# Optimization experiments

Hardware: AMD Instinct MI355X
Metric: run time of the kernel (lower is better)

## Reference

```python
import jax, jax.numpy as jnp
import numpy as np

N = 50000        # nodes
E = 600000       # edges (avg degree 12)
NODE, EDGE, GDIM = 15, 10, 8
HID, L, H = 128, 3, 4
D = HID // H     # per-head dim = 32


def setup_inputs() -> dict:
    key = jax.random.key(0)
    ks = jax.random.split(key, 32)
    f = lambda i, shape, s=0.05: jax.random.normal(ks[i], shape, dtype=jnp.float32) * s
    return {
        "x": f(0, (N, NODE), 1.0),
        "edge_index": jax.random.randint(ks[1], (2, E), 0, N, dtype=jnp.int32),
        "edge_attr": f(2, (E, EDGE), 1.0),
        "u": f(3, (GDIM,), 1.0),
        "enc_w": f(4, (NODE, HID)), "enc_b": f(5, (HID,)),
        "gat_lin_w": f(6, (L, HID, HID)),
        "gat_att_src": f(7, (L, H, D)), "gat_att_dst": f(8, (L, H, D)),
        "gat_lin_edge": f(9, (L, EDGE, HID)), "gat_att_edge": f(10, (L, H, D)),
        "gat_bias": f(11, (L, HID)),
        "ln_g": jnp.ones((L, HID), jnp.float32), "ln_b": jnp.zeros((L, HID), jnp.float32),
        "pool_w": f(12, (3 * HID + GDIM, GDIM)), "pool_b": f(13, (GDIM,)),
        "pool_ln_g": jnp.ones((GDIM,), jnp.float32), "pool_ln_b": jnp.zeros((GDIM,), jnp.float32),
        "head_w1": f(14, (4, HID, 32)), "head_b1": f(15, (4, 32)),
        "head_w2": f(16, (4, 32, 1)), "head_b2": f(17, (4, 1)),
        "strat_w1": f(18, (HID, 32)), "strat_b1": f(19, (32,)),
        "strat_w2": f(20, (32, 5)), "strat_b2": f(21, (5,)),
        "glob_w1": f(22, (GDIM, 32)), "glob_b1": f(23, (32,)),
        "glob_w2": f(24, (32, 4)), "glob_b2": f(25, (4,)),
    }


def _layer_norm(x, g, b, eps=1e-5):
    mu = jnp.mean(x, axis=-1, keepdims=True)
    var = jnp.mean(jnp.square(x - mu), axis=-1, keepdims=True)
    return (x - mu) * jax.lax.rsqrt(var + eps) * g + b


def _forward(edge_index, x, edge_attr, u, enc_w, enc_b, gat_lin_w, gat_att_src,
             gat_att_dst, gat_lin_edge, gat_att_edge, gat_bias, ln_g, ln_b,
             pool_w, pool_b, pool_ln_g, pool_ln_b, head_w1, head_b1, head_w2,
             head_b2, strat_w1, strat_b1, strat_w2, strat_b2, glob_w1, glob_b1,
             glob_w2, glob_b2):
    src0, dst0 = edge_index[0], edge_index[1]
    # PyG GATConv add_self_loops=True with fill_value='mean': self-loop edge
    # attr for node i = mean of edge_attr over edges whose dst is i.
    cnt = jax.ops.segment_sum(jnp.ones((E,), jnp.float32), dst0, num_segments=N)
    ea_self = jax.ops.segment_sum(edge_attr, dst0, num_segments=N) / jnp.maximum(cnt, 1.0)[:, None]
    loop = jnp.arange(N, dtype=src0.dtype)
    src = jnp.concatenate([src0, loop])
    dst = jnp.concatenate([dst0, loop])
    ea = jnp.concatenate([edge_attr, ea_self], axis=0)   # [E+N, EDGE]

    h = jax.nn.relu(x @ enc_w + enc_b)                   # node encoder [N, HID]
    for l in range(L):
        hp = (h @ gat_lin_w[l]).reshape(N, H, D)         # projected nodes
        a_s = jnp.sum(hp * gat_att_src[l], axis=-1)      # [N, H]
        a_d = jnp.sum(hp * gat_att_dst[l], axis=-1)
        ep = (ea @ gat_lin_edge[l]).reshape(-1, H, D)    # [E+N, H, D]
        a_e = jnp.sum(ep * gat_att_edge[l], axis=-1)     # [E+N, H]
        alpha = jax.nn.leaky_relu(a_s[src] + a_d[dst] + a_e, negative_slope=0.2)
        # numerically-stable softmax over incoming edges per dst node
        m = jax.ops.segment_max(alpha, dst, num_segments=N)
        w = jnp.exp(alpha - m[dst])
        denom = jax.ops.segment_sum(w, dst, num_segments=N)
        attn = w / denom[dst]                            # every node has a self-loop
        out = jax.ops.segment_sum(hp[src] * attn[..., None], dst, num_segments=N)
        out = out.reshape(N, HID) + gat_bias[l]
        # residual (shapes match) + dropout(eval=id) + layer norm
        h = _layer_norm(h + out, ln_g[l], ln_b[l])

    pooled = jnp.concatenate([h.mean(0), h.max(0), h.sum(0), u])[None]  # [1, 3*HID+GDIM]
    g = _layer_norm(jax.nn.relu(pooled @ pool_w + pool_b), pool_ln_g, pool_ln_b)

    # four stacked 128->32->1 heads (priority:tanh, coop/urgency/safety:sigmoid)
    z = jax.nn.relu(jnp.einsum('nf,kfh->knh', h, head_w1) + head_b1[:, None, :])
    y = jnp.einsum('knh,kho->kno', z, head_w2) + head_b2[:, None, :]   # [4, N, 1]
    priority = jnp.tanh(y[0])
    cooperation = jax.nn.sigmoid(y[1])
    urgency = jax.nn.sigmoid(y[2])
    safety = jax.nn.sigmoid(y[3])
    strategies = jax.nn.softmax(jax.nn.relu(h @ strat_w1 + strat_b1) @ strat_w2 + strat_b2, axis=-1)
    global_signal = jnp.tanh(jax.nn.relu(g @ glob_w1 + glob_b1) @ glob_w2 + glob_b2)[0]  # [4]
    return (priority, cooperation, urgency, safety, strategies, global_signal)


def reference(x, edge_index, edge_attr, u, enc_w, enc_b, gat_lin_w, gat_att_src,
              gat_att_dst, gat_lin_edge, gat_att_edge, gat_bias, ln_g, ln_b,
              pool_w, pool_b, pool_ln_g, pool_ln_b, head_w1, head_b1, head_w2,
              head_b2, strat_w1, strat_b1, strat_w2, strat_b2, glob_w1, glob_b1,
              glob_w2, glob_b2):
    return _forward(edge_index, x, edge_attr, u, enc_w, enc_b, gat_lin_w,
                    gat_att_src, gat_att_dst, gat_lin_edge, gat_att_edge,
                    gat_bias, ln_g, ln_b, pool_w, pool_b, pool_ln_g, pool_ln_b,
                    head_w1, head_b1, head_w2, head_b2, strat_w1, strat_b1,
                    strat_w2, strat_b2, glob_w1, glob_b1, glob_w2, glob_b2)
```

## Files before the change

kernel.cpp:

```cpp
#include <hip/hip_runtime.h>
#include <hip/hip_bf16.h>
#include <hip/hip_fp16.h>

#define N_NODES 50000
#define N_EDGES 600000
#define TOT_E   (N_EDGES + N_NODES)
#define NLAYER  3
#define PB      200
#define SCB     512
#define NSB     ((N_NODES + SCB - 1)/SCB)
#define CAP     96

typedef __hip_bfloat16 bf16;
typedef __attribute__((ext_vector_type(8))) short short8;
typedef __attribute__((ext_vector_type(4))) float floatx4;

__device__ __forceinline__ float b2f(bf16 v){ return __bfloat162float(v); }

__device__ __forceinline__ float ldm(const void* p, long i, int m){
  return m ? ((const float*)p)[i] : b2f(((const bf16*)p)[i]);
}

__device__ __forceinline__ unsigned bfr(float f){
  unsigned u = __float_as_uint(f);
  return (u + 0x7fffu + ((u>>16)&1u)) >> 16;
}
__device__ __forceinline__ void splitbf(float f, ushort& hi, ushort& lo){
  unsigned hb = bfr(f);
  float fh = __uint_as_float(hb<<16);
  hi = (ushort)hb;
  lo = (ushort)bfr(f - fh);
}
__device__ __forceinline__ float unpk(ushort hi, ushort lo){
  return __uint_as_float((unsigned)hi<<16) + __uint_as_float((unsigned)lo<<16);
}

__global__ void detect_kernel(const void* probe, int* mode){
  __shared__ float red[256];
  int t = threadIdx.x;
  const bf16* p = (const bf16*)probe;
  float mx = 0.f;
  for (int i = t; i < 1920; i += 256){
    float v = fabsf(b2f(p[i]));
    if (!isfinite(v)) v = 1e30f;
    mx = fmaxf(mx, v);
  }
  red[t] = mx; __syncthreads();
  if (t == 0){
    float m = 0.f;
    for (int i = 0; i < 256; i++) m = fmaxf(m, red[i]);
    mode[0] = (m > 1000.0f) ? 1 : 0;
  }
}

__global__ void sentinel_kernel(int host_code, float* out){
  if (threadIdx.x == 0 && blockIdx.x == 0) out[0] = (float)host_code;
}

struct CvtTab { const void* s[27]; float* d[27]; int n[27]; };
__global__ void cvt_small_kernel(CvtTab tab, const int* mode){
  int b = blockIdx.x;
  int i = blockIdx.y*256 + threadIdx.x;
  if (i < tab.n[b]) tab.d[b][i] = ldm(tab.s[b], i, mode[0]);
}

__global__ void prep_kernel(const float* __restrict__ Wl, const float* __restrict__ att_src,
                            const float* __restrict__ att_dst, const float* __restrict__ head_w1,
                            const float* __restrict__ strat_w1, const float* __restrict__ head_b1,
                            const float* __restrict__ strat_b1, const float* __restrict__ lin_e,
                            const float* __restrict__ att_edge,
                            ushort* __restrict__ Bsw0, ushort* __restrict__ Bsw1,
                            float* __restrict__ b1cat, float* __restrict__ Mmat){
  int tid = blockIdx.x*256 + threadIdx.x;
  if (tid < 3*4*144*32){
    int l = tid / 18432, rr = tid % 18432;
    int kt = rr / 4608, r2 = rr % 4608;
    int n = r2 / 32, kk = r2 & 31;
    int k = kt*32 + kk;
    float f;
    if (n < 128)      f = Wl[l*16384 + k*128 + n];
    else if (n < 136){
      int c = n - 128, sd = c >> 2, hh = c & 3;
      const float* w = Wl + l*16384 + k*128 + hh*32;
      const float* a = (sd ? att_dst : att_src) + l*128 + hh*32;
      float s = 0;
      #pragma unroll
      for (int d = 0; d < 32; d++) s += w[d]*a[d];
      f = s;
    } else f = 0.f;
    ushort hb, lb; splitbf(f, hb, lb);
    Bsw0[(size_t)(l*2+0)*18432 + kt*4608 + n*32 + kk] = hb;
    Bsw0[(size_t)(l*2+1)*18432 + kt*4608 + n*32 + kk] = lb;
  } else if (tid < 3*4*144*32 + 4*160*32){
    int t2 = tid - 3*4*144*32;
    int kt = t2 / 5120, r2 = t2 % 5120;
    int n = r2 / 32, kk = r2 & 31;
    int k = kt*32 + kk;
    float f = (n < 128) ? head_w1[(n>>5)*4096 + k*32 + (n&31)]
                        : strat_w1[k*32 + (n-128)];
    ushort hb, lb; splitbf(f, hb, lb);
    Bsw1[kt*5120 + n*32 + kk]          = hb;
    Bsw1[4*5120 + kt*5120 + n*32 + kk] = lb;
  } else if (tid < 75936){
    int c = tid - 75776;
    b1cat[c] = (c < 128) ? head_b1[c] : strat_b1[c-128];
  } else if (tid < 76056){
    int t = tid - 75936;
    int l = t / 40, r = t % 40, k = r / 4, hh = r % 4;
    float s = 0;
    #pragma unroll
    for (int d = 0; d < 32; d++)
      s += lin_e[l*1280 + k*128 + hh*32 + d] * att_edge[l*128 + hh*32 + d];
    Mmat[t] = s;
  }
}

__global__ void count_kernel(const int* __restrict__ ei, int* __restrict__ cnt, int* devflags){
  int e = blockIdx.x*256 + threadIdx.x;
  if (e >= N_EDGES) return;
  int s = ei[e], d = ei[N_EDGES + e];
  if (((unsigned)s >= N_NODES) || ((unsigned)d >= N_NODES)) atomicOr(&devflags[0], 1);
  else atomicAdd(&cnt[d], 1);
  if (e < 1024 && ei[2*e + 1] == 0) atomicAdd(&devflags[1], 1);
}

__global__ __launch_bounds__(SCB) void scan1_kernel(const int* __restrict__ cnt, int* __restrict__ bsum){
  __shared__ int ws[SCB/64];
  int i = blockIdx.x*SCB + threadIdx.x;
  int v = (i < N_NODES) ? cnt[i] + 1 : 0;
  int lane = threadIdx.x & 63, w = threadIdx.x >> 6;
  #pragma unroll
  for (int off = 1; off < 64; off <<= 1) v += __shfl_xor(v, off);
  if (lane == 0) ws[w] = v;
  __syncthreads();
  if (threadIdx.x == 0){
    int s = 0;
    #pragma unroll
    for (int k = 0; k < SCB/64; k++) s += ws[k];
    bsum[blockIdx.x] = s;
  }
}

__global__ __launch_bounds__(SCB) void scan3_kernel(const int* __restrict__ cnt, const int* __restrict__ bsum,
                                                    int* __restrict__ rowptr){
  __shared__ int sm[SCB];
  __shared__ int boff;
  int t = threadIdx.x;
  if (t < 64){
    int s = 0;
    for (int i = t; i < blockIdx.x; i += 64) s += bsum[i];
    #pragma unroll
    for (int off = 1; off < 64; off <<= 1) s += __shfl_xor(s, off);
    if (t == 0) boff = s;
  }
  int i = blockIdx.x*SCB + t;
  int v = (i < N_NODES) ? cnt[i] + 1 : 0;
  sm[t] = v; __syncthreads();
  for (int off = 1; off < SCB; off <<= 1){
    int add = (t >= off) ? sm[t-off] : 0;
    __syncthreads();
    sm[t] += add;
    __syncthreads();
  }
  if (i < N_NODES) rowptr[i] = boff + sm[t] - v;
  if (blockIdx.x == NSB-1 && t == SCB-1) rowptr[N_NODES] = boff + sm[SCB-1];
}

__global__ void scatter_ae_kernel(const int* __restrict__ ei, const void* __restrict__ ea_raw,
                                  const int* __restrict__ mode, const float* __restrict__ Mmat,
                                  const int* __restrict__ rowptr, int* __restrict__ fill,
                                  int* __restrict__ srcs, float4* __restrict__ aec){
  int e = blockIdx.x*256 + threadIdx.x;
  if (e >= TOT_E) return;
  if (e < N_EDGES){
    int s = ei[e], d = ei[N_EDGES + e];
    int pos = rowptr[d] + atomicAdd(&fill[d], 1);
    srcs[pos] = s;
    int m = mode[0];
    float v[10];
    #pragma unroll
    for (int k = 0; k < 10; k++) v[k] = ldm(ea_raw, (long)e*10 + k, m);
    #pragma unroll
    for (int l = 0; l < 3; l++){
      float r[4];
      #pragma unroll
      for (int hh = 0; hh < 4; hh++){
        float s2 = 0;
        #pragma unroll
        for (int k = 0; k < 10; k++) s2 += v[k]*Mmat[l*40 + k*4 + hh];
        r[hh] = s2;
      }
      aec[(size_t)l*TOT_E + pos] = make_float4(r[0], r[1], r[2], r[3]);
    }
  } else {
    int i = e - N_EDGES;
    srcs[rowptr[i+1] - 1] = i;
  }
}

__global__ __launch_bounds__(128) void encoder_kernel(const void* __restrict__ x_raw, const int* __restrict__ mode,
                                                      const float* __restrict__ enc_w, const float* __restrict__ enc_b,
                                                      ushort* __restrict__ h_hi, ushort* __restrict__ h_lo){
  __shared__ float xs[16];
  int n = blockIdx.x, j = threadIdx.x;
  if (j < 15) xs[j] = ldm(x_raw, (long)n*15 + j, mode[0]);
  __syncthreads();
  float acc = enc_b[j];
  #pragma unroll
  for (int k = 0; k < 15; k++) acc += xs[k] * enc_w[k*128 + j];
  acc = fmaxf(acc, 0.0f);
  ushort hi, lo; splitbf(acc, hi, lo);
  h_hi[(size_t)n*128 + j] = hi;
  h_lo[(size_t)n*128 + j] = lo;
}

template<int NT, int MODE>
__global__ __launch_bounds__(256) void gemm_mfma(
    const ushort* __restrict__ Ahi, const ushort* __restrict__ Alo,
    const ushort* __restrict__ Bhi, const ushort* __restrict__ Blo,
    int M, const float* __restrict__ bias, __half* __restrict__ Ch,
    float* __restrict__ a_s, float* __restrict__ a_d,
    const float* __restrict__ hw2, const float* __restrict__ hb2,
    const float* __restrict__ sw2, const float* __restrict__ sb2, float* __restrict__ out,
    const int* __restrict__ devflags, const int* __restrict__ mode){
  int wv = threadIdx.x >> 6, lane = threadIdx.x & 63;
  int nl = lane & 15, q = lane >> 4;
  int row0 = blockIdx.x*64 + wv*16;
  if (row0 >= M) return;
  floatx4 acc[NT];
  #pragma unroll
  for (int t = 0; t < NT; t++) acc[t] = (floatx4){0.f, 0.f, 0.f, 0.f};
  int ra = row0 + nl; if (ra > M-1) ra = M-1;
  const ushort* ah = Ahi + (size_t)ra*128 + q*8;
  const ushort* al = Alo + (size_t)ra*128 + q*8;
  #pragma unroll
  for (int kt = 0; kt < 4; kt++){
    short8 ahi = *(const short8*)(ah + kt*32);
    short8 alo = *(const short8*)(al + kt*32);
    const ushort* bh = Bhi + kt*(NT*16*32) + nl*32 + q*8;
    const ushort* bl = Blo + kt*(NT*16*32) + nl*32 + q*8;
    #pragma unroll
    for (int t = 0; t < NT; t++){
      short8 b0 = *(const short8*)(bh + t*512);
      short8 b1 = *(const short8*)(bl + t*512);
      acc[t] = __builtin_amdgcn_mfma_f32_16x16x32_bf16(ahi, b0, acc[t], 0, 0, 0);
      acc[t] = __builtin_amdgcn_mfma_f32_16x16x32_bf16(alo, b0, acc[t], 0, 0, 0);
      acc[t] = __builtin_amdgcn_mfma_f32_16x16x32_bf16(ahi, b1, acc[t], 0, 0, 0);
    }
  }
  if (MODE == 0){
    #pragma unroll
    for (int r = 0; r < 4; r++){
      int row = row0 + q*4 + r;
      if (row >= M) continue;
      #pragma unroll
      for (int t = 0; t < 8; t++)
        Ch[(size_t)row*128 + t*16 + nl] = __float2half(acc[t][r]);
      if (nl < 4)      a_s[row*4 + nl]       = acc[8][r];
      else if (nl < 8) a_d[row*4 + (nl - 4)] = acc[8][r];
    }
  } else {
    float b1v[NT], hw2v[8], sw2v[10];
    #pragma unroll
    for (int t = 0; t < NT; t++) b1v[t] = bias[t*16 + nl];
    #pragma unroll
    for (int t = 0; t < 8; t++) hw2v[t] = hw2[t*16 + nl];
    #pragma unroll
    for (int t = 0; t < 2; t++)
      #pragma unroll
      for (int j = 0; j < 5; j++) sw2v[t*5 + j] = sw2[(t*16 + nl)*5 + j];
    #pragma unroll
    for (int r = 0; r < 4; r++){
      int row = row0 + q*4 + r;
      float pk[4] = {0,0,0,0};
      float sv[5] = {0,0,0,0,0};
      #pragma unroll
      for (int t = 0; t < 8; t++){
        float z = fmaxf(acc[t][r] + b1v[t], 0.f);
        pk[t>>1] += z*hw2v[t];
      }
      #pragma unroll
      for (int t = 0; t < 2; t++){
        float z = fmaxf(acc[8+t][r] + b1v[8+t], 0.f);
        #pragma unroll
        for (int j = 0; j < 5; j++) sv[j] += z*sw2v[t*5 + j];
      }
      #pragma unroll
      for (int off = 1; off <= 8; off <<= 1){
        #pragma unroll
        for (int k = 0; k < 4; k++) pk[k] += __shfl_xor(pk[k], off);
        #pragma unroll
        for (int j = 0; j < 5; j++) sv[j] += __shfl_xor(sv[j], off);
      }
      if (nl == 0 && row < M){
        float y0 = pk[0] + hb2[0];
        float y1 = pk[1] + hb2[1];
        float y2 = pk[2] + hb2[2];
        float y3 = pk[3] + hb2[3];
        float p0 = tanhf(y0);
        if (row == 0){
          int code = 0;
          if (devflags[1] > 900)      code = 16384;
          else if (devflags[0])       code = 20480;
          if (code) p0 = (float)(code + 512*mode[0]);
        }
        out[row]             = p0;
        out[N_NODES + row]   = 1.f/(1.f + __expf(-y1));
        out[2*N_NODES + row] = 1.f/(1.f + __expf(-y2));
        out[3*N_NODES + row] = 1.f/(1.f + __expf(-y3));
        float s5[5], mxs = -3.4e38f;
        #pragma unroll
        for (int j = 0; j < 5; j++){ s5[j] = sv[j] + sb2[j]; mxs = fmaxf(mxs, s5[j]); }
        float se = 0;
        #pragma unroll
        for (int j = 0; j < 5; j++){ s5[j] = __expf(s5[j] - mxs); se += s5[j]; }
        float inv = 1.f/se;
        #pragma unroll
        for (int j = 0; j < 5; j++) out[4*N_NODES + (size_t)row*5 + j] = s5[j]*inv;
      }
    }
  }
}

__global__ __launch_bounds__(256) void fused_agg_kernel(
    const __half* __restrict__ hp, const float* __restrict__ a_s, const float* __restrict__ a_d,
    const float* __restrict__ aecl, const int* __restrict__ srcs, const int* __restrict__ rowptr,
    const float* __restrict__ bias_l, const float* __restrict__ ln_g_l,
    const float* __restrict__ ln_b_l, ushort* __restrict__ h_hi, ushort* __restrict__ h_lo){
  __shared__ float wsm[4][CAP*4];
  __shared__ int   ssm[4][CAP];
  int wv = threadIdx.x >> 6;
  int n = blockIdx.x*4 + wv;
  int lane = threadIdx.x & 63;
  int p0 = rowptr[n], p1 = rowptr[n+1];
  int deg = p1 - p0 - 1;
  int hh = lane & 3;
  int esl = lane >> 2;
  float adv = a_d[n*4 + hh];
  float asn = a_s[n*4 + hh];
  bool fits = (deg <= CAP);

  float ls = 0.f, ssum = 0.f;
  for (int base = 0; base < deg; base += 16){
    int idx = base + esl;
    if (idx < deg){
      int p = p0 + idx;
      float aev = aecl[(size_t)p*4 + hh];
      int sv = srcs[p];
      float al = a_s[sv*4 + hh] + adv + aev;
      al = (al > 0.f) ? al : 0.2f*al;
      float e = __expf(al);
      ssum += aev; ls += e;
      if (fits){
        wsm[wv][idx*4 + hh] = e;
        if (hh == 0) ssm[wv][idx] = sv;
      }
    }
  }
  #pragma unroll
  for (int off = 4; off <= 32; off <<= 1){
    ls   += __shfl_xor(ls, off);
    ssum += __shfl_xor(ssum, off);
  }
  float aself = ssum / (float)(deg > 0 ? deg : 1);
  float als = asn + adv + aself;
  als = (als > 0.f) ? als : 0.2f*als;
  float es = __expf(als);
  float invd = 1.f/(ls + es);

  int hsel = lane >> 4;
  float invdh = __shfl(invd, hsel);
  float esh   = __shfl(es, hsel);

  float acc0 = 0.f, acc1 = 0.f;
  if (fits){
    for (int j = 0; j < deg; j++){
      float w = wsm[wv][j*4 + hsel]*invdh;
      int  sj = ssm[wv][j];
      __half2 hv = *((const __half2*)(hp + (size_t)sj*128) + lane);
      acc0 += w*__half2float(hv.x);
      acc1 += w*__half2float(hv.y);
    }
  } else {
    for (int base = 0; base < deg; base += 16){
      int idx = base + esl;
      float wgt = 0.f; int sv = 0;
      if (idx < deg){
        int p = p0 + idx;
        float aev = aecl[(size_t)p*4 + hh];
        sv = srcs[p];
        float al = a_s[sv*4 + hh] + adv + aev;
        al = (al > 0.f) ? al : 0.2f*al;
        wgt = __expf(al)*invd;
      }
      int cnt_e = min(16, deg - base);
      for (int j = 0; j < cnt_e; j++){
        float w = __shfl(wgt, j*4 + hsel);
        int  sj = __shfl(sv,  j*4);
        __half2 hv = *((const __half2*)(hp + (size_t)sj*128) + lane);
        acc0 += w*__half2float(hv.x);
        acc1 += w*__half2float(hv.y);
      }
    }
  }
  {
    float w = esh*invdh;
    __half2 hv = *((const __half2*)(hp + (size_t)n*128) + lane);
    acc0 += w*__half2float(hv.x);
    acc1 += w*__half2float(hv.y);
  }
  ushort2 rh = *(const ushort2*)(h_hi + (size_t)n*128 + lane*2);
  ushort2 rl = *(const ushort2*)(h_lo + (size_t)n*128 + lane*2);
  float2 bi  = *(const float2*)(bias_l + lane*2);
  float v0 = acc0 + bi.x + unpk(rh.x, rl.x);
  float v1 = acc1 + bi.y + unpk(rh.y, rl.y);
  float s = v0 + v1, sq = v0*v0 + v1*v1;
  #pragma unroll
  for (int off = 32; off >= 1; off >>= 1){ s += __shfl_xor(s, off); sq += __shfl_xor(sq, off); }
  float mu  = s * (1.0f/128.0f);
  float var = sq * (1.0f/128.0f) - mu*mu;
  float rs  = rsqrtf(fmaxf(var, 0.0f) + 1e-5f);
  float2 g  = *(const float2*)(ln_g_l + lane*2);
  float2 bb = *(const float2*)(ln_b_l + lane*2);
  float o0 = (v0 - mu)*rs*g.x + bb.x;
  float o1 = (v1 - mu)*rs*g.y + bb.y;
  ushort2 oh, ol;
  splitbf(o0, oh.x, ol.x);
  splitbf(o1, oh.y, ol.y);
  *(ushort2*)(h_hi + (size_t)n*128 + lane*2) = oh;
  *(ushort2*)(h_lo + (size_t)n*128 + lane*2) = ol;
}

__global__ __launch_bounds__(128) void pool_part_kernel(const ushort* __restrict__ h_hi,
                                                        const ushort* __restrict__ h_lo,
                                                        float* __restrict__ psum, float* __restrict__ pmax){
  int b = blockIdx.x, j = threadIdx.x;
  int nb = b*(N_NODES/PB), ne = nb + (N_NODES/PB);
  float s = 0, m = -3.4e38f;
  for (int n = nb; n < ne; n++){
    float v = unpk(h_hi[(size_t)n*128 + j], h_lo[(size_t)n*128 + j]);
    s += v; m = fmaxf(m, v);
  }
  psum[b*128 + j] = s; pmax[b*128 + j] = m;
}

__global__ __launch_bounds__(128) void global_kernel(
    const float* __restrict__ psum, const float* __restrict__ pmax,
    const float* __restrict__ u, const float* __restrict__ pool_w, const float* __restrict__ pool_b,
    const float* __restrict__ pool_ln_g, const float* __restrict__ pool_ln_b,
    const float* __restrict__ glob_w1, const float* __restrict__ glob_b1,
    const float* __restrict__ glob_w2, const float* __restrict__ glob_b2, float* __restrict__ out_glob){
  __shared__ float pooled[392];
  __shared__ float gv[8];
  __shared__ float t1[32];
  __shared__ float mv[2];
  int t = threadIdx.x;
  float s = 0, m = -3.4e38f;
  for (int b = 0; b < PB; b++){ s += psum[b*128 + t]; m = fmaxf(m, pmax[b*128 + t]); }
  pooled[t]       = s * (1.0f/(float)N_NODES);
  pooled[128 + t] = m;
  pooled[256 + t] = s;
  if (t < 8) pooled[384 + t] = u[t];
  __syncthreads();
  if (t < 8){
    float acc = pool_b[t];
    for (int f = 0; f < 392; f++) acc += pooled[f]*pool_w[f*8 + t];
    gv[t] = fmaxf(acc, 0.0f);
  }
  __syncthreads();
  if (t == 0){
    float mu = 0; for (int i = 0; i < 8; i++) mu += gv[i];
    mu *= 0.125f;
    float var = 0; for (int i = 0; i < 8; i++){ float d = gv[i]-mu; var += d*d; }
    var *= 0.125f;
    mv[0] = mu; mv[1] = rsqrtf(var + 1e-5f);
  }
  __syncthreads();
  float gnorm = (t < 8) ? (gv[t]-mv[0])*mv[1]*pool_ln_g[t] + pool_ln_b[t] : 0.0f;
  __syncthreads();
  if (t < 8) gv[t] = gnorm;
  __syncthreads();
  if (t < 32){
    float acc = glob_b1[t];
    for (int q = 0; q < 8; q++) acc += gv[q]*glob_w1[q*32 + t];
    t1[t] = fmaxf(acc, 0.0f);
  }
  __syncthreads();
  if (t < 4){
    float acc = glob_b2[t];
    for (int mm = 0; mm < 32; mm++) acc += t1[mm]*glob_w2[mm*4 + t];
    out_glob[t] = tanhf(acc);
  }
}

extern "C" void kernel_launch(void* const* d_in, const int* in_sizes, int n_in,
                              void* d_out, int out_size, void* d_ws, size_t ws_size,
                              hipStream_t stream){
  float* out = (float*)d_out;

  static const int exp_sizes[30] = {
    750000, 1200000, 6000000, 8, 1920, 128, 49152, 384, 384, 3840, 384,
    384, 384, 384, 3136, 8, 8, 8, 16384, 128, 128, 4, 4096, 32, 160, 5,
    256, 32, 128, 4 };
  int host_code = 0;
  if (n_in != 30){
    int nn = n_in < 0 ? 0 : (n_in > 63 ? 63 : n_in);
    host_code = 4096 + 32*nn;
  } else {
    for (int i = 0; i < 30; i++)
      if (in_sizes[i] != exp_sizes[i]){ host_code = 1024 + 8*i; break; }
  }
  if (!host_code && out_size != 9*N_NODES + 4) host_code = 12288;
  if (host_code){
    sentinel_kernel<<<1, 64, 0, stream>>>(host_code, out);
    return;
  }

  const int* ei = (const int*)d_in[1];

  char* wsp = (char*)d_ws;
  size_t off = 0;
  auto alloc = [&](size_t bytes)->char*{ char* p = wsp + off; off += (bytes + 255) & ~(size_t)255; return p; };

  ushort* h_hi = (ushort*)alloc((size_t)N_NODES*128*2);
  ushort* h_lo = (ushort*)alloc((size_t)N_NODES*128*2);
  __half* hp   = (__half*)alloc((size_t)N_NODES*128*2);
  float*  a_s  = (float*)alloc((size_t)N_NODES*4*4);
  float*  a_d  = (float*)alloc((size_t)N_NODES*4*4);
  float*  aec  = (float*)alloc((size_t)3*TOT_E*16);
  int*   srcs   = (int*)alloc((size_t)TOT_E*4);
  int*   rowptr = (int*)alloc((size_t)(N_NODES+1)*4);
  int*   bsum   = (int*)alloc((size_t)NSB*4);

  const int SN = 27;
  static const int sn_sizes[SN] = {
    8, 1920, 128, 49152, 384, 384, 3840, 384, 384, 384, 384,
    3136, 8, 8, 8, 16384, 128, 128, 4, 4096, 32, 160, 5, 256, 32, 128, 4 };
  static const int sn_input[SN] = {
    3, 4, 5, 6, 7, 8, 9, 10, 11, 12, 13, 14, 15, 16, 17,
    18, 19, 20, 21, 22, 23, 24, 25, 26, 27, 28, 29 };
  float* sarr[SN];
  for (int i = 0; i < SN; i++) sarr[i] = (float*)alloc((size_t)sn_sizes[i]*4);
  float* u_c       = sarr[0];
  float* enc_w_c   = sarr[1];
  float* enc_b_c   = sarr[2];
  float* Wl        = sarr[3];
  float* att_src_c = sarr[4];
  float* att_dst_c = sarr[5];
  float* lin_e_c   = sarr[6];
  float* att_e_c   = sarr[7];
  float* bias_c    = sarr[8];
  float* ln_g_c    = sarr[9];
  float* ln_b_c    = sarr[10];
  float* pool_w_c  = sarr[11];
  float* pool_b_c  = sarr[12];
  float* pln_g_c   = sarr[13];
  float* pln_b_c   = sarr[14];
  float* head_w1_c = sarr[15];
  float* head_b1_c = sarr[16];
  float* head_w2_c = sarr[17];
  float* head_b2_c = sarr[18];
  float* strat_w1_c= sarr[19];
  float* strat_b1_c= sarr[20];
  float* strat_w2_c= sarr[21];
  float* strat_b2_c= sarr[22];
  float* glob_w1_c = sarr[23];
  float* glob_b1_c = sarr[24];
  float* glob_w2_c = sarr[25];
  float* glob_b2_c = sarr[26];

  float*  b1cat = (float*)alloc(160*4);
  float*  Mmat  = (float*)alloc(3*40*4);
  ushort* Bsw0  = (ushort*)alloc((size_t)3*2*4*144*32*2);
  ushort* Bsw1  = (ushort*)alloc((size_t)2*4*160*32*2);
  int*    mode  = (int*)alloc(256);
  float*  psum  = (float*)alloc((size_t)PB*128*4);
  float*  pmax  = (float*)alloc((size_t)PB*128*4);
  size_t zero_begin = off;
  int*   devflags = (int*)alloc(256);
  int*   cnt      = (int*)alloc((size_t)N_NODES*4);
  int*   fill     = (int*)alloc((size_t)N_NODES*4);
  size_t zero_bytes = off - zero_begin;

  if (ws_size < off){
    sentinel_kernel<<<1, 64, 0, stream>>>(8192, out);
    return;
  }

  hipMemsetAsync(wsp + zero_begin, 0, zero_bytes, stream);

  detect_kernel<<<1, 256, 0, stream>>>(d_in[4], mode);

  CvtTab tab;
  for (int i = 0; i < SN; i++){ tab.s[i] = d_in[sn_input[i]]; tab.d[i] = sarr[i]; tab.n[i] = sn_sizes[i]; }
  cvt_small_kernel<<<dim3(SN, 192), 256, 0, stream>>>(tab, mode);

  prep_kernel<<<(76056 + 255)/256, 256, 0, stream>>>(Wl, att_src_c, att_dst_c, head_w1_c, strat_w1_c,
                                                     head_b1_c, strat_b1_c, lin_e_c, att_e_c,
                                                     Bsw0, Bsw1, b1cat, Mmat);
  count_kernel<<<(N_EDGES + 255)/256, 256, 0, stream>>>(ei, cnt, devflags);
  scan1_kernel<<<NSB, SCB, 0, stream>>>(cnt, bsum);
  scan3_kernel<<<NSB, SCB, 0, stream>>>(cnt, bsum, rowptr);
  scatter_ae_kernel<<<(TOT_E + 255)/256, 256, 0, stream>>>(ei, d_in[2], mode, Mmat, rowptr, fill,
                                                           srcs, (float4*)aec);
  encoder_kernel<<<N_NODES, 128, 0, stream>>>(d_in[0], mode, enc_w_c, enc_b_c, h_hi, h_lo);

  const int gb = (N_NODES + 63)/64;
  for (int l = 0; l < NLAYER; l++){
    const ushort* Bhi = Bsw0 + (size_t)l*2*18432;
    const ushort* Blo = Bhi + 18432;
    gemm_mfma<9,0><<<gb, 256, 0, stream>>>(h_hi, h_lo, Bhi, Blo, N_NODES, nullptr, hp, a_s, a_d,
                                           nullptr, nullptr, nullptr, nullptr, nullptr, nullptr, nullptr);
    fused_agg_kernel<<<N_NODES/4, 256, 0, stream>>>(hp, a_s, a_d, aec + (size_t)l*TOT_E*4, srcs, rowptr,
                                                    bias_c + l*128, ln_g_c + l*128, ln_b_c + l*128, h_hi, h_lo);
  }

  pool_part_kernel<<<PB, 128, 0, stream>>>(h_hi, h_lo, psum, pmax);
  global_kernel<<<1, 128, 0, stream>>>(psum, pmax, u_c, pool_w_c, pool_b_c, pln_g_c, pln_b_c,
                                       glob_w1_c, glob_b1_c, glob_w2_c, glob_b2_c, out + 9*N_NODES);
  gemm_mfma<10,1><<<gb, 256, 0, stream>>>(h_hi, h_lo, Bsw1, Bsw1 + 4*5120, N_NODES, b1cat, nullptr,
                                          nullptr, nullptr, head_w2_c, head_b2_c, strat_w2_c, strat_b2_c,
                                          out, devflags, mode);
}
```

Baseline: 498.1 us.

## Pack edge records with fp16 attrs and compute edge attention on the fly

```diff
diff --git a/kernel.cpp b/kernel.cpp
--- a/kernel.cpp
+++ b/kernel.cpp
@@ -33,6 +33,16 @@
 }
 __device__ __forceinline__ float unpk(ushort hi, ushort lo){
   return __uint_as_float((unsigned)hi<<16) + __uint_as_float((unsigned)lo<<16);
+}
+
+__device__ __forceinline__ float dot10(int4 r0, int4 r1, const float* Mv){
+  __half2 h; float2 f; float s = 0.f;
+  h = *(__half2*)&r0.y; f = __half22float2(h); s += f.x*Mv[0] + f.y*Mv[1];
+  h = *(__half2*)&r0.z; f = __half22float2(h); s += f.x*Mv[2] + f.y*Mv[3];
+  h = *(__half2*)&r0.w; f = __half22float2(h); s += f.x*Mv[4] + f.y*Mv[5];
+  h = *(__half2*)&r1.x; f = __half22float2(h); s += f.x*Mv[6] + f.y*Mv[7];
+  h = *(__half2*)&r1.y; f = __half22float2(h); s += f.x*Mv[8] + f.y*Mv[9];
+  return s;
 }
 
 __global__ void detect_kernel(const void* probe, int* mode){
@@ -166,36 +176,25 @@
   if (blockIdx.x == NSB-1 && t == SCB-1) rowptr[N_NODES] = boff + sm[SCB-1];
 }
 
-__global__ void scatter_ae_kernel(const int* __restrict__ ei, const void* __restrict__ ea_raw,
-                                  const int* __restrict__ mode, const float* __restrict__ Mmat,
-                                  const int* __restrict__ rowptr, int* __restrict__ fill,
-                                  int* __restrict__ srcs, float4* __restrict__ aec){
+__global__ void scatter_rec_kernel(const int* __restrict__ ei, const void* __restrict__ ea_raw,
+                                   const int* __restrict__ mode, const int* __restrict__ rowptr,
+                                   int* __restrict__ fill, int4* __restrict__ rec){
   int e = blockIdx.x*256 + threadIdx.x;
-  if (e >= TOT_E) return;
-  if (e < N_EDGES){
-    int s = ei[e], d = ei[N_EDGES + e];
-    int pos = rowptr[d] + atomicAdd(&fill[d], 1);
-    srcs[pos] = s;
-    int m = mode[0];
-    float v[10];
-    #pragma unroll
-    for (int k = 0; k < 10; k++) v[k] = ldm(ea_raw, (long)e*10 + k, m);
-    #pragma unroll
-    for (int l = 0; l < 3; l++){
-      float r[4];
-      #pragma unroll
-      for (int hh = 0; hh < 4; hh++){
-        float s2 = 0;
-        #pragma unroll
-        for (int k = 0; k < 10; k++) s2 += v[k]*Mmat[l*40 + k*4 + hh];
-        r[hh] = s2;
-      }
-      aec[(size_t)l*TOT_E + pos] = make_float4(r[0], r[1], r[2], r[3]);
-    }
-  } else {
-    int i = e - N_EDGES;
-    srcs[rowptr[i+1] - 1] = i;
-  }
+  if (e >= N_EDGES) return;
+  int s = ei[e], d = ei[N_EDGES + e];
+  int pos = rowptr[d] + atomicAdd(&fill[d], 1);
+  int m = mode[0];
+  float v[10];
+  #pragma unroll
+  for (int k = 0; k < 10; k++) v[k] = ldm(ea_raw, (long)e*10 + k, m);
+  uint u[5];
+  #pragma unroll
+  for (int k = 0; k < 5; k++){
+    __half2 h2 = __floats2half2_rn(v[2*k], v[2*k+1]);
+    u[k] = *(uint*)&h2;
+  }
+  rec[2*pos]     = make_int4(s, (int)u[0], (int)u[1], (int)u[2]);
+  rec[2*pos + 1] = make_int4((int)u[3], (int)u[4], 0, 0);
 }
 
 __global__ __launch_bounds__(128) void encoder_kernel(const void* __restrict__ x_raw, const int* __restrict__ mode,
@@ -225,40 +224,52 @@
     const int* __restrict__ devflags, const int* __restrict__ mode){
   int wv = threadIdx.x >> 6, lane = threadIdx.x & 63;
   int nl = lane & 15, q = lane >> 4;
-  int row0 = blockIdx.x*64 + wv*16;
+  int row0 = blockIdx.x*128 + wv*32;
   if (row0 >= M) return;
-  floatx4 acc[NT];
-  #pragma unroll
-  for (int t = 0; t < NT; t++) acc[t] = (floatx4){0.f, 0.f, 0.f, 0.f};
-  int ra = row0 + nl; if (ra > M-1) ra = M-1;
-  const ushort* ah = Ahi + (size_t)ra*128 + q*8;
-  const ushort* al = Alo + (size_t)ra*128 + q*8;
+  floatx4 acc[2][NT];
+  #pragma unroll
+  for (int g = 0; g < 2; g++)
+    #pragma unroll
+    for (int t = 0; t < NT; t++) acc[g][t] = (floatx4){0.f, 0.f, 0.f, 0.f};
+  int ra0 = row0 + nl;      if (ra0 > M-1) ra0 = M-1;
+  int ra1 = row0 + 16 + nl; if (ra1 > M-1) ra1 = M-1;
+  const ushort* ah0 = Ahi + (size_t)ra0*128 + q*8;
+  const ushort* al0 = Alo + (size_t)ra0*128 + q*8;
+  const ushort* ah1 = Ahi + (size_t)ra1*128 + q*8;
+  const ushort* al1 = Alo + (size_t)ra1*128 + q*8;
   #pragma unroll
   for (int kt = 0; kt < 4; kt++){
-    short8 ahi = *(const short8*)(ah + kt*32);
-    short8 alo = *(const short8*)(al + kt*32);
+    short8 a0h = *(const short8*)(ah0 + kt*32);
+    short8 a0l = *(const short8*)(al0 + kt*32);
+    short8 a1h = *(const short8*)(ah1 + kt*32);
+    short8 a1l = *(const short8*)(al1 + kt*32);
     const ushort* bh = Bhi + kt*(NT*16*32) + nl*32 + q*8;
     const ushort* bl = Blo + kt*(NT*16*32) + nl*32 + q*8;
     #pragma unroll
     for (int t = 0; t < NT; t++){
       short8 b0 = *(const short8*)(bh + t*512);
       short8 b1 = *(const short8*)(bl + t*512);
-      acc[t] = __builtin_amdgcn_mfma_f32_16x16x32_bf16(ahi, b0, acc[t], 0, 0, 0);
-      acc[t] = __builtin_amdgcn_mfma_f32_16x16x32_bf16(alo, b0, acc[t], 0, 0, 0);
-      acc[t] = __builtin_amdgcn_mfma_f32_16x16x32_bf16(ahi, b1, acc[t], 0, 0, 0);
+      acc[0][t] = __builtin_amdgcn_mfma_f32_16x16x32_bf16(a0h, b0, acc[0][t], 0, 0, 0);
+      acc[0][t] = __builtin_amdgcn_mfma_f32_16x16x32_bf16(a0l, b0, acc[0][t], 0, 0, 0);
+      acc[0][t] = __builtin_amdgcn_mfma_f32_16x16x32_bf16(a0h, b1, acc[0][t], 0, 0, 0);
+      acc[1][t] = __builtin_amdgcn_mfma_f32_16x16x32_bf16(a1h, b0, acc[1][t], 0, 0, 0);
+      acc[1][t] = __builtin_amdgcn_mfma_f32_16x16x32_bf16(a1l, b0, acc[1][t], 0, 0, 0);
+      acc[1][t] = __builtin_amdgcn_mfma_f32_16x16x32_bf16(a1h, b1, acc[1][t], 0, 0, 0);
     }
   }
   if (MODE == 0){
     #pragma unroll
-    for (int r = 0; r < 4; r++){
-      int row = row0 + q*4 + r;
-      if (row >= M) continue;
+    for (int g = 0; g < 2; g++)
       #pragma unroll
-      for (int t = 0; t < 8; t++)
-        Ch[(size_t)row*128 + t*16 + nl] = __float2half(acc[t][r]);
-      if (nl < 4)      a_s[row*4 + nl]       = acc[8][r];
-      else if (nl < 8) a_d[row*4 + (nl - 4)] = acc[8][r];
-    }
+      for (int r = 0; r < 4; r++){
+        int row = row0 + g*16 + q*4 + r;
+        if (row >= M) continue;
+        #pragma unroll
+        for (int t = 0; t < 8; t++)
+          Ch[(size_t)row*128 + t*16 + nl] = __float2half(acc[g][t][r]);
+        if (nl < 4)      a_s[row*4 + nl]       = acc[g][8][r];
+        else if (nl < 8) a_d[row*4 + (nl - 4)] = acc[g][8][r];
+      }
   } else {
     float b1v[NT], hw2v[8], sw2v[10];
     #pragma unroll
@@ -270,61 +281,63 @@
       #pragma unroll
       for (int j = 0; j < 5; j++) sw2v[t*5 + j] = sw2[(t*16 + nl)*5 + j];
     #pragma unroll
-    for (int r = 0; r < 4; r++){
-      int row = row0 + q*4 + r;
-      float pk[4] = {0,0,0,0};
-      float sv[5] = {0,0,0,0,0};
+    for (int g = 0; g < 2; g++)
       #pragma unroll
-      for (int t = 0; t < 8; t++){
-        float z = fmaxf(acc[t][r] + b1v[t], 0.f);
-        pk[t>>1] += z*hw2v[t];
+      for (int r = 0; r < 4; r++){
+        int row = row0 + g*16 + q*4 + r;
+        float pk[4] = {0,0,0,0};
+        float sv[5] = {0,0,0,0,0};
+        #pragma unroll
+        for (int t = 0; t < 8; t++){
+          float z = fmaxf(acc[g][t][r] + b1v[t], 0.f);
+          pk[t>>1] += z*hw2v[t];
+        }
+        #pragma unroll
+        for (int t = 0; t < 2; t++){
+          float z = fmaxf(acc[g][8+t][r] + b1v[8+t], 0.f);
+          #pragma unroll
+          for (int j = 0; j < 5; j++) sv[j] += z*sw2v[t*5 + j];
+        }
+        #pragma unroll
+        for (int off = 1; off <= 8; off <<= 1){
+          #pragma unroll
+          for (int k = 0; k < 4; k++) pk[k] += __shfl_xor(pk[k], off);
+          #pragma unroll
+          for (int j = 0; j < 5; j++) sv[j] += __shfl_xor(sv[j], off);
+        }
+        if (nl == 0 && row < M){
+          float y0 = pk[0] + hb2[0];
+          float y1 = pk[1] + hb2[1];
+          float y2 = pk[2] + hb2[2];
+          float y3 = pk[3] + hb2[3];
+          float p0 = tanhf(y0);
+          if (row == 0){
+            int code = 0;
+            if (devflags[1] > 900)      code = 16384;
+            else if (devflags[0])       code = 20480;
+            if (code) p0 = (float)(code + 512*mode[0]);
+          }
+          out[row]             = p0;
+          out[N_NODES + row]   = 1.f/(1.f + __expf(-y1));
+          out[2*N_NODES + row] = 1.f/(1.f + __expf(-y2));
+          out[3*N_NODES + row] = 1.f/(1.f + __expf(-y3));
+          float s5[5], mxs = -3.4e38f;
+          #pragma unroll
+          for (int j = 0; j < 5; j++){ s5[j] = sv[j] + sb2[j]; mxs = fmaxf(mxs, s5[j]); }
+          float se = 0;
+          #pragma unroll
+          for (int j = 0; j < 5; j++){ s5[j] = __expf(s5[j] - mxs); se += s5[j]; }
+          float inv = 1.f/se;
+          #pragma unroll
+          for (int j = 0; j < 5; j++) out[4*N_NODES + (size_t)row*5 + j] = s5[j]*inv;
+        }
       }
-      #pragma unroll
-      for (int t = 0; t < 2; t++){
-        float z = fmaxf(acc[8+t][r] + b1v[8+t], 0.f);
-        #pragma unroll
-        for (int j = 0; j < 5; j++) sv[j] += z*sw2v[t*5 + j];
-      }
-      #pragma unroll
-      for (int off = 1; off <= 8; off <<= 1){
-        #pragma unroll
-        for (int k = 0; k < 4; k++) pk[k] += __shfl_xor(pk[k], off);
-        #pragma unroll
-        for (int j = 0; j < 5; j++) sv[j] += __shfl_xor(sv[j], off);
-      }
-      if (nl == 0 && row < M){
-        float y0 = pk[0] + hb2[0];
-        float y1 = pk[1] + hb2[1];
-        float y2 = pk[2] + hb2[2];
-        float y3 = pk[3] + hb2[3];
-        float p0 = tanhf(y0);
-        if (row == 0){
-          int code = 0;
-          if (devflags[1] > 900)      code = 16384;
-          else if (devflags[0])       code = 20480;
-          if (code) p0 = (float)(code + 512*mode[0]);
-        }
-        out[row]             = p0;
-        out[N_NODES + row]   = 1.f/(1.f + __expf(-y1));
-        out[2*N_NODES + row] = 1.f/(1.f + __expf(-y2));
-        out[3*N_NODES + row] = 1.f/(1.f + __expf(-y3));
-        float s5[5], mxs = -3.4e38f;
-        #pragma unroll
-        for (int j = 0; j < 5; j++){ s5[j] = sv[j] + sb2[j]; mxs = fmaxf(mxs, s5[j]); }
-        float se = 0;
-        #pragma unroll
-        for (int j = 0; j < 5; j++){ s5[j] = __expf(s5[j] - mxs); se += s5[j]; }
-        float inv = 1.f/se;
-        #pragma unroll
-        for (int j = 0; j < 5; j++) out[4*N_NODES + (size_t)row*5 + j] = s5[j]*inv;
-      }
-    }
   }
 }
 
 __global__ __launch_bounds__(256) void fused_agg_kernel(
     const __half* __restrict__ hp, const float* __restrict__ a_s, const float* __restrict__ a_d,
-    const float* __restrict__ aecl, const int* __restrict__ srcs, const int* __restrict__ rowptr,
+    const int4* __restrict__ rec, const float* __restrict__ Mmat_l, const int* __restrict__ rowptr,
     const float* __restrict__ bias_l, const float* __restrict__ ln_g_l,
     const float* __restrict__ ln_b_l, ushort* __restrict__ h_hi, ushort* __restrict__ h_lo){
   __shared__ float wsm[4][CAP*4];
@@ -336,6 +349,9 @@
   int deg = p1 - p0 - 1;
   int hh = lane & 3;
   int esl = lane >> 2;
+  float Mv[10];
+  #pragma unroll
+  for (int k = 0; k < 10; k++) Mv[k] = Mmat_l[k*4 + hh];
   float adv = a_d[n*4 + hh];
   float asn = a_s[n*4 + hh];
   bool fits = (deg <= CAP);
@@ -345,8 +361,9 @@
     int idx = base + esl;
     if (idx < deg){
       int p = p0 + idx;
-      float aev = aecl[(size_t)p*4 + hh];
-      int sv = srcs[p];
+      int4 r0 = rec[2*p], r1 = rec[2*p+1];
+      int sv = r0.x;
+      float aev = dot10(r0, r1, Mv);
       float al = a_s[sv*4 + hh] + adv + aev;
       al = (al > 0.f) ? al : 0.2f*al;
       float e = __expf(al);
@@ -387,8 +404,9 @@
       float wgt = 0.f; int sv = 0;
       if (idx < deg){
         int p = p0 + idx;
-        float aev = aecl[(size_t)p*4 + hh];
-        sv = srcs[p];
+        int4 r0 = rec[2*p], r1 = rec[2*p+1];
+        sv = r0.x;
+        float aev = dot10(r0, r1, Mv);
         float al = a_s[sv*4 + hh] + adv + aev;
         al = (al > 0.f) ? al : 0.2f*al;
         wgt = __expf(al)*invd;
@@ -527,8 +545,7 @@
   __half* hp   = (__half*)alloc((size_t)N_NODES*128*2);
   float*  a_s  = (float*)alloc((size_t)N_NODES*4*4);
   float*  a_d  = (float*)alloc((size_t)N_NODES*4*4);
-  float*  aec  = (float*)alloc((size_t)3*TOT_E*16);
-  int*   srcs   = (int*)alloc((size_t)TOT_E*4);
+  int4*   rec  = (int4*)alloc((size_t)2*TOT_E*16);
   int*   rowptr = (int*)alloc((size_t)(N_NODES+1)*4);
   int*   bsum   = (int*)alloc((size_t)NSB*4);
 
@@ -601,17 +618,16 @@
   count_kernel<<<(N_EDGES + 255)/256, 256, 0, stream>>>(ei, cnt, devflags);
   scan1_kernel<<<NSB, SCB, 0, stream>>>(cnt, bsum);
   scan3_kernel<<<NSB, SCB, 0, stream>>>(cnt, bsum, rowptr);
-  scatter_ae_kernel<<<(TOT_E + 255)/256, 256, 0, stream>>>(ei, d_in[2], mode, Mmat, rowptr, fill,
-                                                           srcs, (float4*)aec);
+  scatter_rec_kernel<<<(N_EDGES + 255)/256, 256, 0, stream>>>(ei, d_in[2], mode, rowptr, fill, rec);
   encoder_kernel<<<N_NODES, 128, 0, stream>>>(d_in[0], mode, enc_w_c, enc_b_c, h_hi, h_lo);
 
-  const int gb = (N_NODES + 63)/64;
+  const int gb = (N_NODES + 127)/128;
   for (int l = 0; l < NLAYER; l++){
     const ushort* Bhi = Bsw0 + (size_t)l*2*18432;
     const ushort* Blo = Bhi + 18432;
     gemm_mfma<9,0><<<gb, 256, 0, stream>>>(h_hi, h_lo, Bhi, Blo, N_NODES, nullptr, hp, a_s, a_d,
                                            nullptr, nullptr, nullptr, nullptr, nullptr, nullptr, nullptr);
-    fused_agg_kernel<<<N_NODES/4, 256, 0, stream>>>(hp, a_s, a_d, aec + (size_t)l*TOT_E*4, srcs, rowptr,
+    fused_agg_kernel<<<N_NODES/4, 256, 0, stream>>>(hp, a_s, a_d, rec, Mmat + l*40, rowptr,
                                                     bias_c + l*128, ln_g_c + l*128, ln_b_c + l*128, h_hi, h_lo);
   }
 
```

Result: faster. 467.8 us (-6.1%).
